# Performance work log

Hardware: AMD Instinct MI355X
Metric: run time of the kernel (lower is better)

## Reference

```python
import jax, jax.numpy as jnp
import numpy as np

B, T, D, H, K = 128, 128, 2048, 512, 512
KSIZES = (2, 3, 4, 5)
OUT_DIM = 2048
IN_DIM = 2 * H + len(KSIZES) * K + D  # 5120
BN_EPS = 1e-5


def _gru_dir(x, w_ih, w_hh, b_ih, b_hh):
    """Single-direction torch-style GRU. x: [B,T,D] -> [B,T,H]."""
    xw = jnp.einsum('btd,gd->btg', x, w_ih) + b_ih  # precompute input proj [B,T,3H]
    h0 = jnp.zeros((x.shape[0], w_hh.shape[1]), x.dtype)

    def step(h, xw_t):
        gh = h @ w_hh.T + b_hh
        xr, xz, xn = jnp.split(xw_t, 3, axis=-1)
        hr, hz, hn = jnp.split(gh, 3, axis=-1)
        r = jax.nn.sigmoid(xr + hr)
        z = jax.nn.sigmoid(xz + hz)
        n = jnp.tanh(xn + r * hn)
        h_new = (1.0 - z) * n + z * h
        return h_new, h_new

    _, hs = jax.lax.scan(step, h0, jnp.swapaxes(xw, 0, 1))
    return jnp.swapaxes(hs, 0, 1)


def _forward(videos, videos_origin, videos_mask, lengths,
             w_ih_f, w_hh_f, b_ih_f, b_hh_f,
             w_ih_b, w_hh_b, b_ih_b, b_hh_b,
             conv_w2, conv_b2, conv_w3, conv_b3, conv_w4, conv_b4, conv_w5, conv_b5,
             fc_w, fc_b, bn_gamma, bn_beta, bn_mean, bn_var):
    # bidirectional GRU on the full padded sequence (torch code does NOT pack)
    fwd = _gru_dir(videos, w_ih_f, w_hh_f, b_ih_f, b_hh_f)
    bwd = _gru_dir(videos[:, ::-1], w_ih_b, w_hh_b, b_ih_b, b_hh_b)[:, ::-1]
    gru_init = jnp.concatenate([fwd, bwd], axis=-1)  # [B,T,2H]

    # fused masked mean (replaces per-sample python loop): mean over first lengths[i] steps
    masked = gru_init * videos_mask[:, :, None]
    mean_gru = masked.sum(axis=1) / lengths.astype(gru_init.dtype)[:, None]  # [B,2H]

    # multi-scale text-CNN over masked GRU outputs
    x4 = masked[:, None, :, :]  # [B,1,T,2H]
    cons = []
    for w, cw, cb in zip(KSIZES, (conv_w2, conv_w3, conv_w4, conv_w5),
                         (conv_b2, conv_b3, conv_b4, conv_b5)):
        y = jax.lax.conv_general_dilated(
            x4, cw, window_strides=(1, 1), padding=[(w - 1, w - 1), (0, 0)],
            dimension_numbers=('NCHW', 'OIHW', 'NCHW'))  # [B,K,T+w-1,1]
        y = jax.nn.relu(y + cb[None, :, None, None])
        cons.append(y.max(axis=(2, 3)))  # global max-pool over time
    con_out = jnp.concatenate(cons, axis=1)  # [B, 4K]

    # concate == 'full' ; dropout is identity at inference
    feats = jnp.concatenate([mean_gru, con_out, videos_origin], axis=1)  # [B,5120]
    feats = feats @ fc_w + fc_b
    feats = bn_gamma * (feats - bn_mean) / jnp.sqrt(bn_var + BN_EPS) + bn_beta
    # l2norm over feature dim
    feats = feats / jnp.sqrt(jnp.sum(feats * feats, axis=1, keepdims=True))
    return feats


def setup_inputs() -> dict:
    key = jax.random.key(0)
    ks = jax.random.split(key, 32)
    s = 0.02
    inp = {
        'videos': jax.random.normal(ks[0], (B, T, D), jnp.float32),
        'videos_origin': jax.random.normal(ks[1], (B, D), jnp.float32),
    }
    lengths = jax.random.randint(ks[2], (B,), 1, T + 1).astype(jnp.int64)
    inp['lengths'] = lengths
    inp['videos_mask'] = (jnp.arange(T)[None, :] < lengths[:, None]).astype(jnp.float32)
    inp['w_ih_f'] = jax.random.normal(ks[3], (3 * H, D), jnp.float32) * s
    inp['w_hh_f'] = jax.random.normal(ks[4], (3 * H, H), jnp.float32) * s
    inp['b_ih_f'] = jnp.zeros((3 * H,), jnp.float32)
    inp['b_hh_f'] = jnp.zeros((3 * H,), jnp.float32)
    inp['w_ih_b'] = jax.random.normal(ks[5], (3 * H, D), jnp.float32) * s
    inp['w_hh_b'] = jax.random.normal(ks[6], (3 * H, H), jnp.float32) * s
    inp['b_ih_b'] = jnp.zeros((3 * H,), jnp.float32)
    inp['b_hh_b'] = jnp.zeros((3 * H,), jnp.float32)
    for i, w in enumerate(KSIZES):
        inp[f'conv_w{w}'] = jax.random.normal(ks[7 + i], (K, 1, w, 2 * H), jnp.float32) * s
        inp[f'conv_b{w}'] = jnp.zeros((K,), jnp.float32)
    inp['fc_w'] = jax.random.normal(ks[12], (IN_DIM, OUT_DIM), jnp.float32) * s
    inp['fc_b'] = jnp.zeros((OUT_DIM,), jnp.float32)
    inp['bn_gamma'] = jnp.ones((OUT_DIM,), jnp.float32)
    inp['bn_beta'] = jnp.zeros((OUT_DIM,), jnp.float32)
    inp['bn_mean'] = jnp.zeros((OUT_DIM,), jnp.float32)
    inp['bn_var'] = jnp.ones((OUT_DIM,), jnp.float32)
    return inp


def reference(videos, videos_origin, lengths, videos_mask,
              w_ih_f, w_hh_f, b_ih_f, b_hh_f,
              w_ih_b, w_hh_b, b_ih_b, b_hh_b,
              conv_w2, conv_b2, conv_w3, conv_b3, conv_w4, conv_b4, conv_w5, conv_b5,
              fc_w, fc_b, bn_gamma, bn_beta, bn_mean, bn_var):
    return _forward(videos, videos_origin, videos_mask, lengths,
                    w_ih_f, w_hh_f, b_ih_f, b_hh_f,
                    w_ih_b, w_hh_b, b_ih_b, b_hh_b,
                    conv_w2, conv_b2, conv_w3, conv_b3, conv_w4, conv_b4, conv_w5, conv_b5,
                    fc_w, fc_b, bn_gamma, bn_beta, bn_mean, bn_var)
```

## Files before the change

### kernel.cpp

```cpp
#include <hip/hip_runtime.h>
#include <stdint.h>

#define B_   128
#define T_   128
#define D_   2048
#define H_   512
#define G3   1536
#define CH   1024
#define KC   512
#define OUTD 2048
#define IND  5120
#define TP   168
#define MPAD 160

typedef short vb8 __attribute__((ext_vector_type(8)));
typedef float v4f __attribute__((ext_vector_type(4)));

__device__ __forceinline__ unsigned short f2b(float f) {
  unsigned u = __float_as_uint(f);
  u = (u + 0x7FFFu + ((u >> 16) & 1u)) >> 16;
  return (unsigned short)u;
}
__device__ __forceinline__ float b2f(unsigned short u) {
  return __uint_as_float((unsigned)u << 16);
}

__device__ __forceinline__ void gl16(const unsigned short* g, unsigned short* l) {
  __builtin_amdgcn_global_load_lds(
      (const __attribute__((address_space(1))) void*)g,
      (__attribute__((address_space(3))) void*)l, 16, 0, 0);
}

__global__ void k_cvt(const float* __restrict__ in, unsigned short* __restrict__ out, int n4) {
  int stride = gridDim.x * blockDim.x;
  for (int i = blockIdx.x * blockDim.x + threadIdx.x; i < n4; i += stride) {
    float4 v = reinterpret_cast<const float4*>(in)[i];
    ushort4 o;
    o.x = f2b(v.x); o.y = f2b(v.y); o.z = f2b(v.z); o.w = f2b(v.w);
    reinterpret_cast<ushort4*>(out)[i] = o;
  }
}

__global__ void k_tcvt(const float* __restrict__ in, unsigned short* __restrict__ out) {
  __shared__ float tile[32][33];
  const int tx = threadIdx.x & 31;
  const int ty = threadIdx.x >> 5;
  const int n0 = blockIdx.x * 32;
  const int k0 = blockIdx.y * 32;
#pragma unroll
  for (int i = 0; i < 4; ++i)
    tile[ty + 8 * i][tx] = in[(size_t)(k0 + ty + 8 * i) * OUTD + n0 + tx];
  __syncthreads();
#pragma unroll
  for (int i = 0; i < 4; ++i)
    out[(size_t)(n0 + ty + 8 * i) * IND + k0 + tx] = f2b(tile[tx][ty + 8 * i]);
}

template<int EPI, int CB>
__global__ __launch_bounds__(256) void k_gemm(
    const unsigned short* __restrict__ A,
    const unsigned short* __restrict__ Bm,
    const float* __restrict__ bias,
    void* __restrict__ Cv,
    int K, int lda, int ldc, int convw)
{
  __shared__ unsigned short sA[128 * 32];
  __shared__ unsigned short sB[128 * 32];
  float*          C32 = (float*)Cv;
  unsigned short* C16 = (unsigned short*)Cv;

  const int tid  = threadIdx.x;
  const int lane = tid & 63;
  const int wv   = tid >> 6;
  const int wr   = wv >> 1;
  const int wc   = wv & 1;
  const int m0   = blockIdx.x * 128;
  const int n0   = blockIdx.y * 128;

  const unsigned short* ag[2];
  const unsigned short* bg[2];
  unsigned short* al[2];
  unsigned short* bl[2];
#pragma unroll
  for (int q = 0; q < 2; ++q) {
    int c  = wv * 2 + q;
    int r  = c * 16 + (lane >> 2);
    int kc = (lane & 3) * 8;
    long abase;
    if (EPI == 1) {
      int m   = m0 + r;
      int b   = m / MPAD;
      int tau = m - b * MPAD;
      abase = (long)(b * TP + 4 + tau - (convw - 1)) * CH;
    } else {
      abase = (long)(m0 + r) * lda;
    }
    ag[q] = A + abase + kc;
    bg[q] = Bm + (long)(n0 + r) * K + kc;
    al[q] = sA + c * 512;
    bl[q] = sB + c * 512;
  }

  v4f acc[4][4] = {};
  const int kq = (lane >> 4) * 8;
  const int fr = lane & 15;

  for (int k0 = 0; k0 < K; k0 += 32) {
    if (k0) __syncthreads();
#pragma unroll
    for (int q = 0; q < 2; ++q) {
      gl16(ag[q] + k0, al[q]);
      gl16(bg[q] + k0, bl[q]);
    }
    __syncthreads();
    vb8 af[4], bfr[4];
#pragma unroll
    for (int i = 0; i < 4; ++i) {
      af[i]  = *reinterpret_cast<const vb8*>(sA + (wr * 64 + i * 16 + fr) * 32 + kq);
      bfr[i] = *reinterpret_cast<const vb8*>(sB + (wc * 64 + i * 16 + fr) * 32 + kq);
    }
#pragma unroll
    for (int i = 0; i < 4; ++i)
#pragma unroll
      for (int j = 0; j < 4; ++j)
        acc[i][j] = __builtin_amdgcn_mfma_f32_16x16x32_bf16(af[i], bfr[j], acc[i][j], 0, 0, 0);
  }

  const int rl = lane >> 4;
#pragma unroll
  for (int i = 0; i < 4; ++i) {
#pragma unroll
    for (int j = 0; j < 4; ++j) {
      int col = n0 + wc * 64 + j * 16 + fr;
      float bs = bias[col];
      if (EPI == 0) {
#pragma unroll
        for (int r = 0; r < 4; ++r) {
          int m = m0 + wr * 64 + i * 16 + rl * 4 + r;
          float v = acc[i][j][r] + bs;
          if (CB) C16[(long)m * ldc + col] = f2b(v);
          else    C32[(long)m * ldc + col] = v;
        }
      } else {
        int mf = m0 + wr * 64 + i * 16;
        int b  = mf / MPAD;
        int tf = mf - b * MPAD;
        float mx = 0.f;
#pragma unroll
        for (int r = 0; r < 4; ++r) {
          int tau = tf + rl * 4 + r;
          float v = acc[i][j][r] + bs;
          v = v > 0.f ? v : 0.f;
          if (tau < T_ + convw - 1) mx = v > mx ? v : mx;
        }
        mx = fmaxf(mx, __shfl_xor(mx, 16));
        mx = fmaxf(mx, __shfl_xor(mx, 32));
        if (rl == 0 && tf < T_ + convw - 1)
          atomicMax(reinterpret_cast<int*>(C32 + (long)b * ldc + col), __float_as_int(mx));
      }
    }
  }
}

__global__ __launch_bounds__(512) void k_scan(
    const unsigned short* __restrict__ whh16,
    const float* __restrict__ bhhf, const float* __restrict__ bhhb,
    const unsigned short* __restrict__ xw,
    const int* __restrict__ lengths,
    unsigned short* __restrict__ hbuf,
    unsigned short* __restrict__ xpad,
    float* __restrict__ meang,
    unsigned int* __restrict__ cnt)
{
  __shared__ unsigned short sw[96 * 512];
  const int wg   = blockIdx.x;
  const int dir  = wg >> 4;
  const int u0   = (wg & 15) * 32;
  const int tid  = threadIdx.x;
  const int lane = tid & 63;
  const int wv   = tid >> 6;
  const int fr   = lane & 15;
  const int rl   = lane >> 4;
  const int kq   = rl * 8;

  const unsigned short* Wd  = whh16 + (size_t)dir * (3 * H_ * H_);
  const float*          bhh = dir ? bhhb : bhhf;
  const unsigned short* xwd = xw + (size_t)dir * ((size_t)B_ * T_ * G3);
  unsigned short* hb = hbuf + dir * (2 * B_ * H_);
  unsigned int* mycnt = cnt + dir * 64;

  for (int i = tid; i < 96 * 64; i += 512) {
    int row  = i >> 6;
    int slot = i & 63;
    const unsigned short* src = Wd + (size_t)((row >> 5) * H_ + u0 + (row & 31)) * H_ + slot * 8;
    *reinterpret_cast<vb8*>((char*)sw + ((row * 1024 + slot * 16) ^ ((row & 7) << 4))) =
        *reinterpret_cast<const vb8*>(src);
  }
  __syncthreads();

  int mylen[4];
#pragma unroll
  for (int r = 0; r < 4; ++r) mylen[r] = lengths[wv * 16 + rl * 4 + r];

  float bh[3][2];
#pragma unroll
  for (int g = 0; g < 3; ++g)
#pragma unroll
    for (int j = 0; j < 2; ++j) bh[g][j] = bhh[g * H_ + u0 + j * 16 + fr];

  float hst[8], macc[8];
#pragma unroll
  for (int i = 0; i < 8; ++i) { hst[i] = 0.f; macc[i] = 0.f; }

  unsigned short uxw[3][2][4];
  {
    const int t0 = dir ? (T_ - 1) : 0;
#pragma unroll
    for (int g = 0; g < 3; ++g)
#pragma unroll
      for (int j = 0; j < 2; ++j)
#pragma unroll
        for (int r = 0; r < 4; ++r)
          uxw[g][j][r] = xwd[((size_t)(wv * 16 + rl * 4 + r) * T_ + t0) * G3 +
                             g * H_ + u0 + j * 16 + fr];
  }

  for (int s = 0; s < T_; ++s) {
    const int t = dir ? (T_ - 1 - s) : s;

    v4f acc[3][2] = {};
    if (s > 0) {
      const unsigned short* arow = hb + ((s - 1) & 1) * (B_ * H_) + (wv * 16 + fr) * H_;
#pragma unroll 4
      for (int ks = 0; ks < 16; ++ks) {
        vb8 a = *reinterpret_cast<const vb8*>(arow + ks * 32 + kq);
#pragma unroll
        for (int g = 0; g < 3; ++g)
#pragma unroll
          for (int j = 0; j < 2; ++j) {
            vb8 wf = *reinterpret_cast<const vb8*>(
                (const char*)sw +
                (((g * 32 + j * 16 + fr) * 1024 + ks * 64 + rl * 16) ^ ((fr & 7) << 4)));
            acc[g][j] = __builtin_amdgcn_mfma_f32_16x16x32_bf16(a, wf, acc[g][j], 0, 0, 0);
          }
      }
    }

    unsigned short* hc = hb + (s & 1) * (B_ * H_);
#pragma unroll
    for (int j = 0; j < 2; ++j)
#pragma unroll
      for (int r = 0; r < 4; ++r) {
        const int idx = j * 4 + r;
        const int b   = wv * 16 + rl * 4 + r;
        const int u   = u0 + j * 16 + fr;
        float xr = b2f(uxw[0][j][r]), xz = b2f(uxw[1][j][r]), xn = b2f(uxw[2][j][r]);
        float hr = acc[0][j][r] + bh[0][j];
        float hz = acc[1][j][r] + bh[1][j];
        float hn = acc[2][j][r] + bh[2][j];
        float rr = 1.f / (1.f + __expf(-(xr + hr)));
        float z  = 1.f / (1.f + __expf(-(xz + hz)));
        float ax = xn + rr * hn;
        float n  = 2.f / (1.f + __expf(-2.f * ax)) - 1.f;
        float h  = (1.f - z) * n + z * hst[idx];
        hst[idx] = h;
        hc[b * H_ + u] = f2b(h);
        if (t < mylen[r]) {
          xpad[((size_t)b * TP + 4 + t) * CH + dir * H_ + u] = f2b(h);
          macc[idx] += h;
        }
      }

    if (s < T_ - 1) {
      const int tn = dir ? (T_ - 2 - s) : (s + 1);
#pragma unroll
      for (int g = 0; g < 3; ++g)
#pragma unroll
        for (int j = 0; j < 2; ++j)
#pragma unroll
          for (int r = 0; r < 4; ++r)
            uxw[g][j][r] = xwd[((size_t)(wv * 16 + rl * 4 + r) * T_ + tn) * G3 +
                               g * H_ + u0 + j * 16 + fr];
      __syncthreads();
      if (tid == 0) {
        __hip_atomic_fetch_add(mycnt, 1u, __ATOMIC_RELEASE, __HIP_MEMORY_SCOPE_AGENT);
        const unsigned tgt = (unsigned)(s + 1) * 16;
        while (__hip_atomic_load(mycnt, __ATOMIC_RELAXED, __HIP_MEMORY_SCOPE_AGENT) < tgt)
          __builtin_amdgcn_s_sleep(1);
        __builtin_amdgcn_fence(__ATOMIC_ACQUIRE, "agent");
      }
      __syncthreads();
    }
  }

#pragma unroll
  for (int j = 0; j < 2; ++j)
#pragma unroll
    for (int r = 0; r < 4; ++r)
      meang[(size_t)(wv * 16 + rl * 4 + r) * CH + dir * H_ + u0 + j * 16 + fr] =
          macc[j * 4 + r] / (float)mylen[r];
}

__global__ void k_feats(const float* __restrict__ mg, const float* __restrict__ co,
                        const float* __restrict__ vo, unsigned short* __restrict__ out) {
  int i = blockIdx.x * 256 + threadIdx.x;
  int b = i / IND, c = i - b * IND;
  float v;
  if (c < CH) v = mg[b * CH + c];
  else if (c < CH + OUTD) v = co[b * OUTD + (c - CH)];
  else v = vo[b * D_ + (c - CH - OUTD)];
  out[i] = f2b(v);
}

__global__ __launch_bounds__(256) void k_bnnorm(const float* __restrict__ x,
    const float* __restrict__ g, const float* __restrict__ bt,
    const float* __restrict__ mn, const float* __restrict__ vr,
    float* __restrict__ out) {
  const int b = blockIdx.x;
  __shared__ float red[4];
  float vals[8];
  float ss = 0.f;
#pragma unroll
  for (int i = 0; i < 8; ++i) {
    int c = threadIdx.x + i * 256;
    float y = g[c] * (x[(size_t)b * OUTD + c] - mn[c]) / sqrtf(vr[c] + 1e-5f) + bt[c];
    vals[i] = y;
    ss += y * y;
  }
#pragma unroll
  for (int s2 = 1; s2 < 64; s2 <<= 1) ss += __shfl_xor(ss, s2);
  if ((threadIdx.x & 63) == 0) red[threadIdx.x >> 6] = ss;
  __syncthreads();
  float inv = 1.f / sqrtf(red[0] + red[1] + red[2] + red[3]);
#pragma unroll
  for (int i = 0; i < 8; ++i)
    out[(size_t)b * OUTD + threadIdx.x + i * 256] = vals[i] * inv;
}

extern "C" void kernel_launch(void* const* d_in, const int* in_sizes, int n_in,
                              void* d_out, int out_size, void* d_ws, size_t ws_size,
                              hipStream_t stream) {
  (void)in_sizes; (void)n_in; (void)out_size; (void)ws_size;
  const float* videos = (const float*)d_in[0];
  const float* vorig  = (const float*)d_in[1];
  const int*   lens   = (const int*)d_in[2];
  const float* wihf = (const float*)d_in[4];
  const float* whhf = (const float*)d_in[5];
  const float* bihf = (const float*)d_in[6];
  const float* bhhf = (const float*)d_in[7];
  const float* wihb = (const float*)d_in[8];
  const float* whhb = (const float*)d_in[9];
  const float* bihb = (const float*)d_in[10];
  const float* bhhb = (const float*)d_in[11];
  const float* cw[4] = {(const float*)d_in[12], (const float*)d_in[14],
                        (const float*)d_in[16], (const float*)d_in[18]};
  const float* cb[4] = {(const float*)d_in[13], (const float*)d_in[15],
                        (const float*)d_in[17], (const float*)d_in[19]};
  const float* fcw = (const float*)d_in[20];
  const float* fcb = (const float*)d_in[21];
  const float* bng = (const float*)d_in[22];
  const float* bnb = (const float*)d_in[23];
  const float* bnm = (const float*)d_in[24];
  const float* bnv = (const float*)d_in[25];
  float* out = (float*)d_out;

  char* ws = (char*)d_ws;
  size_t off = 0;
  auto alloc = [&](size_t bytes) -> void* {
    void* p = ws + off;
    off = (off + bytes + 255) & ~(size_t)255;
    return p;
  };
  unsigned int*   cnt    = (unsigned int*)alloc(1024);
  unsigned short* xw16   = (unsigned short*)alloc((size_t)2 * B_ * T_ * G3 * 2);
  unsigned short* whh16  = (unsigned short*)alloc((size_t)2 * 3 * H_ * H_ * 2);
  unsigned short* hbuf   = (unsigned short*)alloc((size_t)2 * 2 * B_ * H_ * 2);
  float*          meang  = (float*)alloc((size_t)B_ * CH * 4);
  float*          conout = (float*)alloc((size_t)B_ * OUTD * 4);
  unsigned short* feats  = (unsigned short*)alloc((size_t)B_ * IND * 2);
  float*          fcout  = (float*)alloc((size_t)B_ * OUTD * 4);
  unsigned short* wihf16 = (unsigned short*)alloc((size_t)G3 * D_ * 2);
  unsigned short* wihb16 = (unsigned short*)alloc((size_t)G3 * D_ * 2);
  unsigned short* cw16   = (unsigned short*)alloc((size_t)KC * 14 * CH * 2);
  unsigned short* vid16  = (unsigned short*)alloc((size_t)B_ * T_ * D_ * 2);
  unsigned short* xpad = vid16;
  unsigned short* fcT  = vid16 + (size_t)B_ * TP * CH;

  hipMemsetAsync(cnt, 0, 1024, stream);
  hipMemsetAsync(conout, 0, (size_t)B_ * OUTD * 4, stream);

  k_cvt<<<2048, 256, 0, stream>>>(videos, vid16, B_ * T_ * D_ / 4);
  k_cvt<<<512, 256, 0, stream>>>(wihf, wihf16, G3 * D_ / 4);
  k_cvt<<<512, 256, 0, stream>>>(wihb, wihb16, G3 * D_ / 4);
  k_cvt<<<768, 256, 0, stream>>>(whhf, whh16, 3 * H_ * H_ / 4);
  k_cvt<<<768, 256, 0, stream>>>(whhb, whh16 + (size_t)3 * H_ * H_, 3 * H_ * H_ / 4);
  {
    size_t cwoff = 0;
    for (int i = 0; i < 4; ++i) {
      int w = i + 2;
      int n = KC * w * CH;
      k_cvt<<<256, 256, 0, stream>>>(cw[i], cw16 + cwoff, n / 4);
      cwoff += (size_t)n;
    }
  }

  k_gemm<0, 1><<<dim3(128, 12), 256, 0, stream>>>(vid16, wihf16, bihf, xw16, D_, D_, G3, 0);
  k_gemm<0, 1><<<dim3(128, 12), 256, 0, stream>>>(vid16, wihb16, bihb,
                                                  xw16 + (size_t)B_ * T_ * G3, D_, D_, G3, 0);

  hipMemsetAsync(xpad, 0, (size_t)B_ * TP * CH * 2, stream);
  k_tcvt<<<dim3(64, 160), 256, 0, stream>>>(fcw, fcT);

  k_scan<<<dim3(32), dim3(512), 0, stream>>>(whh16, bhhf, bhhb, xw16, lens,
                                             hbuf, xpad, meang, cnt);

  {
    size_t cwoff = 0;
    for (int i = 0; i < 4; ++i) {
      int w = i + 2;
      k_gemm<1, 0><<<dim3(160, 4), 256, 0, stream>>>(xpad, cw16 + cwoff, cb[i],
                                                     conout + i * KC, w * CH, 0, OUTD, w);
      cwoff += (size_t)KC * w * CH;
    }
  }

  k_feats<<<2560, 256, 0, stream>>>(meang, conout, vorig, feats);
  k_gemm<0, 0><<<dim3(1, 16), 256, 0, stream>>>(feats, fcT, fcb, fcout, IND, IND, OUTD, 0);
  k_bnnorm<<<B_, 256, 0, stream>>>(fcout, bng, bnb, bnm, bnv, out);
}
```

Measured before the change: 1.940 ms.

## Replace scan grid counter barrier with per-block flags and staged hidden-state stores

```diff
diff --git a/kernel.cpp b/kernel.cpp
--- a/kernel.cpp
+++ b/kernel.cpp
@@ -170,15 +170,18 @@
     unsigned short* __restrict__ hbuf,
     unsigned short* __restrict__ xpad,
     float* __restrict__ meang,
-    unsigned int* __restrict__ cnt)
+    unsigned int* __restrict__ flags)
 {
   __shared__ unsigned short sw[96 * 512];
+  __shared__ unsigned short hstage[128][36];
   const int wg   = blockIdx.x;
   const int dir  = wg >> 4;
   const int u0   = (wg & 15) * 32;
   const int tid  = threadIdx.x;
   const int lane = tid & 63;
   const int wv   = tid >> 6;
+  const int mg   = wv & 3;
+  const int jh   = wv >> 2;
   const int fr   = lane & 15;
   const int rl   = lane >> 4;
   const int kq   = rl * 8;
@@ -187,7 +190,7 @@
   const float*          bhh = dir ? bhhb : bhhf;
   const unsigned short* xwd = xw + (size_t)dir * ((size_t)B_ * T_ * G3);
   unsigned short* hb = hbuf + dir * (2 * B_ * H_);
-  unsigned int* mycnt = cnt + dir * 64;
+  unsigned int* myflags = flags + dir * 16 * 32;
 
   for (int i = tid; i < 96 * 64; i += 512) {
     int row  = i >> 6;
@@ -198,15 +201,18 @@
   }
   __syncthreads();
 
-  int mylen[4];
-#pragma unroll
-  for (int r = 0; r < 4; ++r) mylen[r] = lengths[wv * 16 + rl * 4 + r];
-
-  float bh[3][2];
-#pragma unroll
-  for (int g = 0; g < 3; ++g)
-#pragma unroll
-    for (int j = 0; j < 2; ++j) bh[g][j] = bhh[g * H_ + u0 + j * 16 + fr];
+  const int u = u0 + jh * 16 + fr;
+
+  int mylen[8];
+#pragma unroll
+  for (int mt = 0; mt < 2; ++mt)
+#pragma unroll
+    for (int r = 0; r < 4; ++r)
+      mylen[mt * 4 + r] = lengths[mg * 32 + mt * 16 + rl * 4 + r];
+
+  float bh[3];
+#pragma unroll
+  for (int g = 0; g < 3; ++g) bh[g] = bhh[g * H_ + u];
 
   float hst[8], macc[8];
 #pragma unroll
@@ -218,54 +224,61 @@
 #pragma unroll
     for (int g = 0; g < 3; ++g)
 #pragma unroll
-      for (int j = 0; j < 2; ++j)
+      for (int mt = 0; mt < 2; ++mt)
 #pragma unroll
         for (int r = 0; r < 4; ++r)
-          uxw[g][j][r] = xwd[((size_t)(wv * 16 + rl * 4 + r) * T_ + t0) * G3 +
-                             g * H_ + u0 + j * 16 + fr];
+          uxw[g][mt][r] = xwd[((size_t)(mg * 32 + mt * 16 + rl * 4 + r) * T_ + t0) * G3 +
+                              g * H_ + u];
   }
 
   for (int s = 0; s < T_; ++s) {
     const int t = dir ? (T_ - 1 - s) : s;
 
-    v4f acc[3][2] = {};
+    v4f acc[2][3] = {};
     if (s > 0) {
-      const unsigned short* arow = hb + ((s - 1) & 1) * (B_ * H_) + (wv * 16 + fr) * H_;
-#pragma unroll 4
+      const unsigned short* hp = hb + ((s - 1) & 1) * (B_ * H_);
+#pragma unroll 8
       for (int ks = 0; ks < 16; ++ks) {
-        vb8 a = *reinterpret_cast<const vb8*>(arow + ks * 32 + kq);
-#pragma unroll
-        for (int g = 0; g < 3; ++g)
-#pragma unroll
-          for (int j = 0; j < 2; ++j) {
-            vb8 wf = *reinterpret_cast<const vb8*>(
-                (const char*)sw +
-                (((g * 32 + j * 16 + fr) * 1024 + ks * 64 + rl * 16) ^ ((fr & 7) << 4)));
-            acc[g][j] = __builtin_amdgcn_mfma_f32_16x16x32_bf16(a, wf, acc[g][j], 0, 0, 0);
-          }
+        vb8 a[2];
+#pragma unroll
+        for (int mt = 0; mt < 2; ++mt) {
+          const unsigned long long* ap = reinterpret_cast<const unsigned long long*>(
+              hp + (size_t)(mg * 32 + mt * 16 + fr) * H_ + ks * 32 + kq);
+          unsigned long long l0 = __hip_atomic_load(ap, __ATOMIC_RELAXED, __HIP_MEMORY_SCOPE_AGENT);
+          unsigned long long l1 = __hip_atomic_load(ap + 1, __ATOMIC_RELAXED, __HIP_MEMORY_SCOPE_AGENT);
+          union { unsigned long long q[2]; vb8 v; } U;
+          U.q[0] = l0; U.q[1] = l1;
+          a[mt] = U.v;
+        }
+#pragma unroll
+        for (int g = 0; g < 3; ++g) {
+          const int row = g * 32 + jh * 16 + fr;
+          vb8 wf = *reinterpret_cast<const vb8*>(
+              (const char*)sw + (((row * 1024) + ks * 64 + rl * 16) ^ ((row & 7) << 4)));
+          acc[0][g] = __builtin_amdgcn_mfma_f32_16x16x32_bf16(a[0], wf, acc[0][g], 0, 0, 0);
+          acc[1][g] = __builtin_amdgcn_mfma_f32_16x16x32_bf16(a[1], wf, acc[1][g], 0, 0, 0);
+        }
       }
     }
 
-    unsigned short* hc = hb + (s & 1) * (B_ * H_);
-#pragma unroll
-    for (int j = 0; j < 2; ++j)
+#pragma unroll
+    for (int mt = 0; mt < 2; ++mt)
 #pragma unroll
       for (int r = 0; r < 4; ++r) {
-        const int idx = j * 4 + r;
-        const int b   = wv * 16 + rl * 4 + r;
-        const int u   = u0 + j * 16 + fr;
-        float xr = b2f(uxw[0][j][r]), xz = b2f(uxw[1][j][r]), xn = b2f(uxw[2][j][r]);
-        float hr = acc[0][j][r] + bh[0][j];
-        float hz = acc[1][j][r] + bh[1][j];
-        float hn = acc[2][j][r] + bh[2][j];
+        const int idx = mt * 4 + r;
+        const int b   = mg * 32 + mt * 16 + rl * 4 + r;
+        float xr = b2f(uxw[0][mt][r]), xz = b2f(uxw[1][mt][r]), xn = b2f(uxw[2][mt][r]);
+        float hr = acc[mt][0][r] + bh[0];
+        float hz = acc[mt][1][r] + bh[1];
+        float hn = acc[mt][2][r] + bh[2];
         float rr = 1.f / (1.f + __expf(-(xr + hr)));
         float z  = 1.f / (1.f + __expf(-(xz + hz)));
         float ax = xn + rr * hn;
         float n  = 2.f / (1.f + __expf(-2.f * ax)) - 1.f;
         float h  = (1.f - z) * n + z * hst[idx];
         hst[idx] = h;
-        hc[b * H_ + u] = f2b(h);
-        if (t < mylen[r]) {
+        hstage[b][jh * 16 + fr] = f2b(h);
+        if (t < mylen[idx]) {
           xpad[((size_t)b * TP + 4 + t) * CH + dir * H_ + u] = f2b(h);
           macc[idx] += h;
         }
@@ -276,29 +289,46 @@
 #pragma unroll
       for (int g = 0; g < 3; ++g)
 #pragma unroll
-        for (int j = 0; j < 2; ++j)
+        for (int mt = 0; mt < 2; ++mt)
 #pragma unroll
           for (int r = 0; r < 4; ++r)
-            uxw[g][j][r] = xwd[((size_t)(wv * 16 + rl * 4 + r) * T_ + tn) * G3 +
-                               g * H_ + u0 + j * 16 + fr];
+            uxw[g][mt][r] = xwd[((size_t)(mg * 32 + mt * 16 + rl * 4 + r) * T_ + tn) * G3 +
+                                g * H_ + u];
       __syncthreads();
-      if (tid == 0) {
-        __hip_atomic_fetch_add(mycnt, 1u, __ATOMIC_RELEASE, __HIP_MEMORY_SCOPE_AGENT);
-        const unsigned tgt = (unsigned)(s + 1) * 16;
-        while (__hip_atomic_load(mycnt, __ATOMIC_RELAXED, __HIP_MEMORY_SCOPE_AGENT) < tgt)
-          __builtin_amdgcn_s_sleep(1);
-        __builtin_amdgcn_fence(__ATOMIC_ACQUIRE, "agent");
+      {
+        const int b   = tid >> 2;
+        const int seg = tid & 3;
+        const unsigned short* src = &hstage[b][seg * 8];
+        unsigned long long q0 = *reinterpret_cast<const unsigned long long*>(src);
+        unsigned long long q1 = *reinterpret_cast<const unsigned long long*>(src + 4);
+        unsigned long long* dst = reinterpret_cast<unsigned long long*>(
+            hb + (s & 1) * (B_ * H_) + (size_t)b * H_ + u0 + seg * 8);
+        __hip_atomic_store(dst,     q0, __ATOMIC_RELAXED, __HIP_MEMORY_SCOPE_AGENT);
+        __hip_atomic_store(dst + 1, q1, __ATOMIC_RELAXED, __HIP_MEMORY_SCOPE_AGENT);
       }
       __syncthreads();
-    }
-  }
-
-#pragma unroll
-  for (int j = 0; j < 2; ++j)
+      asm volatile("" ::: "memory");
+      if (wv == 0) {
+        if (lane == 0)
+          __hip_atomic_store(&myflags[(wg & 15) * 32], (unsigned)(s + 1),
+                             __ATOMIC_RELEASE, __HIP_MEMORY_SCOPE_AGENT);
+        if (lane < 16) {
+          while (__hip_atomic_load(&myflags[lane * 32], __ATOMIC_RELAXED,
+                                   __HIP_MEMORY_SCOPE_AGENT) < (unsigned)(s + 1))
+            __builtin_amdgcn_s_sleep(1);
+        }
+      }
+      asm volatile("" ::: "memory");
+      __syncthreads();
+    }
+  }
+
+#pragma unroll
+  for (int mt = 0; mt < 2; ++mt)
 #pragma unroll
     for (int r = 0; r < 4; ++r)
-      meang[(size_t)(wv * 16 + rl * 4 + r) * CH + dir * H_ + u0 + j * 16 + fr] =
-          macc[j * 4 + r] / (float)mylen[r];
+      meang[(size_t)(mg * 32 + mt * 16 + rl * 4 + r) * CH + dir * H_ + u] =
+          macc[mt * 4 + r] / (float)mylen[mt * 4 + r];
 }
 
 __global__ void k_feats(const float* __restrict__ mg, const float* __restrict__ co,
@@ -371,7 +401,7 @@
     off = (off + bytes + 255) & ~(size_t)255;
     return p;
   };
-  unsigned int*   cnt    = (unsigned int*)alloc(1024);
+  unsigned int*   flags  = (unsigned int*)alloc(4096);
   unsigned short* xw16   = (unsigned short*)alloc((size_t)2 * B_ * T_ * G3 * 2);
   unsigned short* whh16  = (unsigned short*)alloc((size_t)2 * 3 * H_ * H_ * 2);
   unsigned short* hbuf   = (unsigned short*)alloc((size_t)2 * 2 * B_ * H_ * 2);
@@ -386,7 +416,7 @@
   unsigned short* xpad = vid16;
   unsigned short* fcT  = vid16 + (size_t)B_ * TP * CH;
 
-  hipMemsetAsync(cnt, 0, 1024, stream);
+  hipMemsetAsync(flags, 0, 4096, stream);
   hipMemsetAsync(conout, 0, (size_t)B_ * OUTD * 4, stream);
 
   k_cvt<<<2048, 256, 0, stream>>>(videos, vid16, B_ * T_ * D_ / 4);
@@ -412,7 +442,7 @@
   k_tcvt<<<dim3(64, 160), 256, 0, stream>>>(fcw, fcT);
 
   k_scan<<<dim3(32), dim3(512), 0, stream>>>(whh16, bhhf, bhhb, xw16, lens,
-                                             hbuf, xpad, meang, cnt);
+                                             hbuf, xpad, meang, flags);
 
   {
     size_t cwoff = 0;
```

Result: slower. 3.170 ms (+63.4%).

## Merge forward/backward input-projection GEMMs and add XCD-aware block swizzle

Applied to the files above, without the earlier changes.

```diff
diff --git a/kernel.cpp b/kernel.cpp
--- a/kernel.cpp
+++ b/kernel.cpp
@@ -12,6 +12,7 @@
 #define IND  5120
 #define TP   168
 #define MPAD 160
+#define SROW 520
 
 typedef short vb8 __attribute__((ext_vector_type(8)));
 typedef float v4f __attribute__((ext_vector_type(4)));
@@ -69,13 +70,18 @@
   float*          C32 = (float*)Cv;
   unsigned short* C16 = (unsigned short*)Cv;
 
+  const int nwg = gridDim.x * gridDim.y;
+  const int bid = blockIdx.y * gridDim.x + blockIdx.x;
+  const int cpx = nwg >> 3;
+  const int swz = (bid & 7) * cpx + (bid >> 3);
+  const int m0  = (swz % gridDim.x) * 128;
+  const int n0  = (swz / gridDim.x) * 128;
+
   const int tid  = threadIdx.x;
   const int lane = tid & 63;
   const int wv   = tid >> 6;
   const int wr   = wv >> 1;
   const int wc   = wv & 1;
-  const int m0   = blockIdx.x * 128;
-  const int n0   = blockIdx.y * 128;
 
   const unsigned short* ag[2];
   const unsigned short* bg[2];
@@ -140,6 +146,15 @@
           float v = acc[i][j][r] + bs;
           if (CB) C16[(long)m * ldc + col] = f2b(v);
           else    C32[(long)m * ldc + col] = v;
+        }
+      } else if (EPI == 2) {
+        const int dirb = col >= G3;
+        const int xcol = col - dirb * G3;
+        unsigned short* base = C16 + (size_t)dirb * ((size_t)B_ * T_ * G3);
+#pragma unroll
+        for (int r = 0; r < 4; ++r) {
+          int m = m0 + wr * 64 + i * 16 + rl * 4 + r;
+          base[(long)m * G3 + xcol] = f2b(acc[i][j][r] + bs);
         }
       } else {
         int mf = m0 + wr * 64 + i * 16;
@@ -372,6 +387,7 @@
     return p;
   };
   unsigned int*   cnt    = (unsigned int*)alloc(1024);
+  float*          biascat= (float*)alloc(2 * G3 * 4);
   unsigned short* xw16   = (unsigned short*)alloc((size_t)2 * B_ * T_ * G3 * 2);
   unsigned short* whh16  = (unsigned short*)alloc((size_t)2 * 3 * H_ * H_ * 2);
   unsigned short* hbuf   = (unsigned short*)alloc((size_t)2 * 2 * B_ * H_ * 2);
@@ -379,8 +395,7 @@
   float*          conout = (float*)alloc((size_t)B_ * OUTD * 4);
   unsigned short* feats  = (unsigned short*)alloc((size_t)B_ * IND * 2);
   float*          fcout  = (float*)alloc((size_t)B_ * OUTD * 4);
-  unsigned short* wihf16 = (unsigned short*)alloc((size_t)G3 * D_ * 2);
-  unsigned short* wihb16 = (unsigned short*)alloc((size_t)G3 * D_ * 2);
+  unsigned short* wihcat = (unsigned short*)alloc((size_t)2 * G3 * D_ * 2);
   unsigned short* cw16   = (unsigned short*)alloc((size_t)KC * 14 * CH * 2);
   unsigned short* vid16  = (unsigned short*)alloc((size_t)B_ * T_ * D_ * 2);
   unsigned short* xpad = vid16;
@@ -388,10 +403,12 @@
 
   hipMemsetAsync(cnt, 0, 1024, stream);
   hipMemsetAsync(conout, 0, (size_t)B_ * OUTD * 4, stream);
+  hipMemcpyAsync(biascat,      bihf, G3 * 4, hipMemcpyDeviceToDevice, stream);
+  hipMemcpyAsync(biascat + G3, bihb, G3 * 4, hipMemcpyDeviceToDevice, stream);
 
   k_cvt<<<2048, 256, 0, stream>>>(videos, vid16, B_ * T_ * D_ / 4);
-  k_cvt<<<512, 256, 0, stream>>>(wihf, wihf16, G3 * D_ / 4);
-  k_cvt<<<512, 256, 0, stream>>>(wihb, wihb16, G3 * D_ / 4);
+  k_cvt<<<512, 256, 0, stream>>>(wihf, wihcat, G3 * D_ / 4);
+  k_cvt<<<512, 256, 0, stream>>>(wihb, wihcat + (size_t)G3 * D_, G3 * D_ / 4);
   k_cvt<<<768, 256, 0, stream>>>(whhf, whh16, 3 * H_ * H_ / 4);
   k_cvt<<<768, 256, 0, stream>>>(whhb, whh16 + (size_t)3 * H_ * H_, 3 * H_ * H_ / 4);
   {
@@ -404,9 +421,7 @@
     }
   }
 
-  k_gemm<0, 1><<<dim3(128, 12), 256, 0, stream>>>(vid16, wihf16, bihf, xw16, D_, D_, G3, 0);
-  k_gemm<0, 1><<<dim3(128, 12), 256, 0, stream>>>(vid16, wihb16, bihb,
-                                                  xw16 + (size_t)B_ * T_ * G3, D_, D_, G3, 0);
+  k_gemm<2, 1><<<dim3(128, 24), 256, 0, stream>>>(vid16, wihcat, biascat, xw16, D_, D_, 0, 0);
 
   hipMemsetAsync(xpad, 0, (size_t)B_ * TP * CH * 2, stream);
   k_tcvt<<<dim3(64, 160), 256, 0, stream>>>(fcw, fcT);
```

New measurement: 2.056 ms. 1.06x slower.
